# Kernel tuning notes

Hardware: AMD Instinct MI355X
Metric: run time of the kernel (lower is better)

The kernel has to match this reference:

```python
import jax, jax.numpy as jnp
import numpy as np
from jax import lax

B, S, IN, D, E, NH = 8, 128, 512, 1024, 4, 16
DH = D // NH
EPS = 1e-5
SCALE = np.float32(1.0 / np.sqrt(DH))


def setup_inputs() -> dict:
    key = jax.random.key(0)
    ks = iter(jax.random.split(key, 64))
    def rn(shape, scale=0.02):
        return jax.random.normal(next(ks), shape, dtype=jnp.float32) * scale
    z = lambda shape: jnp.zeros(shape, dtype=jnp.float32)
    return {
        "x": jax.random.normal(next(ks), (B, S, IN), dtype=jnp.float32),
        "router_w": rn((IN, E)), "router_b": z((E,)),
        "enc_w1": rn((E, IN, D)), "enc_b1": z((E, D)),
        "enc_w2": rn((E, D, D)), "enc_b2": z((E, D)),
        "enc_g": jnp.ones((E, D), jnp.float32), "enc_beta": z((E, D)),
        "attn_in_w": rn((E, D, 3 * D)), "attn_in_b": z((E, 3 * D)),
        "attn_out_w": rn((E, D, D)), "attn_out_b": z((E, D)),
        "lstm_wi_f": rn((E, D, 4 * D)), "lstm_wh_f": rn((E, D, 4 * D)), "lstm_b_f": z((E, 4 * D)),
        "lstm_wi_b": rn((E, D, 4 * D)), "lstm_wh_b": rn((E, D, 4 * D)), "lstm_b_b": z((E, 4 * D)),
        "sig_w1": rn((E, 2 * D, D)), "sig_b1": z((E, D)),
        "sig_w2": rn((E, D, D)), "sig_b2": z((E, D)),
        "tan_w1": rn((E, 2 * D, D)), "tan_b1": z((E, D)),
        "tan_w2": rn((E, D, D)), "tan_b2": z((E, D)),
        "dec_w1": rn((E, D, D)), "dec_b1": z((E, D)),
        "dec_w2": rn((E, D, IN)), "dec_b2": z((E, IN)),
        "dec_g": jnp.ones((E, IN), jnp.float32), "dec_beta": z((E, IN)),
    }


def _ln(x, g, b):
    m = x.mean(-1, keepdims=True)
    v = ((x - m) ** 2).mean(-1, keepdims=True)
    return (x - m) * lax.rsqrt(v + EPS) * g + b


def _lstm_dir(x, Wi, Wh, b):
    # x: [B,S,D]; single-direction LSTM, returns h sequence [B,S,H]
    bsz = x.shape[0]
    h0 = jnp.zeros((bsz, Wh.shape[0]), x.dtype)
    def step(carry, xt):
        h, c = carry
        zg = xt @ Wi + h @ Wh + b  # [B,4H]; torch gate order i,f,g,o
        i, f, g, o = jnp.split(zg, 4, axis=-1)
        c = jax.nn.sigmoid(f) * c + jax.nn.sigmoid(i) * jnp.tanh(g)
        h = jax.nn.sigmoid(o) * jnp.tanh(c)
        return (h, c), h
    _, hs = lax.scan(step, (h0, h0), jnp.swapaxes(x, 0, 1))
    return jnp.swapaxes(hs, 0, 1)


def _expert(x, p):
    (ew1, eb1, ew2, eb2, eg, ebeta, aiw, aib, aow, aob,
     wif, whf, bf, wibk, whbk, bbk, sw1, sb1, sw2, sb2,
     tw1, tb1, tw2, tb2, dw1, db1, dw2, db2, dg, dbeta) = p
    # encoder MLP + LayerNorm
    h = _ln(jax.nn.relu(x @ ew1 + eb1) @ ew2 + eb2, eg, ebeta)  # [B,S,D]
    # full self-attention (torch MultiheadAttention)
    qkv = h @ aiw + aib
    q, k, v = jnp.split(qkv, 3, axis=-1)
    def heads(t):
        return t.reshape(t.shape[0], t.shape[1], NH, DH).transpose(0, 2, 1, 3)
    q, k, v = heads(q), heads(k), heads(v)
    attn = jax.nn.softmax(jnp.einsum('bhqd,bhkd->bhqk', q, k) * SCALE, axis=-1)
    o = jnp.einsum('bhqk,bhkd->bhqd', attn, v).transpose(0, 2, 1, 3).reshape(h.shape)
    h = o @ aow + aob
    # bidirectional LSTM memory
    hf = _lstm_dir(h, wif, whf, bf)
    hb = _lstm_dir(h[:, ::-1], wibk, whbk, bbk)[:, ::-1]
    mem = jnp.concatenate([hf, hb], axis=-1)  # [B,S,2D]
    # sigmoid/tanh gate branches multiplied
    gate_s = jax.nn.sigmoid(jax.nn.relu(mem @ sw1 + sb1) @ sw2 + sb2)
    gate_t = jnp.tanh(jax.nn.relu(mem @ tw1 + tb1) @ tw2 + tb2)
    g = gate_s * gate_t  # [B,S,D]
    # decoder MLP + LayerNorm back to input_dim
    return _ln(jax.nn.relu(g @ dw1 + db1) @ dw2 + db2, dg, dbeta)


def _forward(x, router_w, router_b, *p):
    outs = jax.vmap(lambda pe: _expert(x, pe))(tuple(p))  # [E,B,S,IN]
    w = jax.nn.softmax(x @ router_w + router_b, axis=-1)  # [B,S,E] token-level routing
    return jnp.einsum('ebsd,bse->bsd', outs, w)


def reference(x, router_w, router_b, enc_w1, enc_b1, enc_w2, enc_b2, enc_g, enc_beta,
              attn_in_w, attn_in_b, attn_out_w, attn_out_b,
              lstm_wi_f, lstm_wh_f, lstm_b_f, lstm_wi_b, lstm_wh_b, lstm_b_b,
              sig_w1, sig_b1, sig_w2, sig_b2, tan_w1, tan_b1, tan_w2, tan_b2,
              dec_w1, dec_b1, dec_w2, dec_b2, dec_g, dec_beta):
    return _forward(x, router_w, router_b, enc_w1, enc_b1, enc_w2, enc_b2, enc_g, enc_beta,
                    attn_in_w, attn_in_b, attn_out_w, attn_out_b,
                    lstm_wi_f, lstm_wh_f, lstm_b_f, lstm_wi_b, lstm_wh_b, lstm_b_b,
                    sig_w1, sig_b1, sig_w2, sig_b2, tan_w1, tan_b1, tan_w2, tan_b2,
                    dec_w1, dec_b1, dec_w2, dec_b2, dec_g, dec_beta)
```

## Files before the change

### kernel.cpp

```cpp
#include <hip/hip_runtime.h>


typedef __attribute__((ext_vector_type(8))) short short8v;
typedef __attribute__((ext_vector_type(4))) float float4v;

__device__ __forceinline__ float bf2f(unsigned short u) {
    unsigned int x = ((unsigned int)u) << 16;
    return __builtin_bit_cast(float, x);
}
__device__ __forceinline__ unsigned short f2bf(float f) {
    unsigned int u = __builtin_bit_cast(unsigned int, f);
    u += 0x7fffu + ((u >> 16) & 1u);
    return (unsigned short)(u >> 16);
}
__device__ __forceinline__ void gload_lds16(const unsigned short* g, unsigned short* lds) {
    __builtin_amdgcn_global_load_lds(
        (const __attribute__((address_space(1))) unsigned int*)g,
        (__attribute__((address_space(3))) unsigned int*)lds, 16, 0, 0);
}
__device__ __forceinline__ float ftanh(float x) {
    float e = __expf(2.f * x);
    return 1.f - 2.f / (e + 1.f);
}

__global__ __launch_bounds__(256) void cvt_bf16_kernel(
    const float* __restrict__ in, unsigned short* __restrict__ out, int n4)
{
    int i = blockIdx.x * 256 + threadIdx.x;
    if (i >= n4) return;
    float4 v = *reinterpret_cast<const float4*>(&in[i * 4]);
    ushort4 o;
    o.x = f2bf(v.x); o.y = f2bf(v.y); o.z = f2bf(v.z); o.w = f2bf(v.w);
    *reinterpret_cast<ushort4*>(&out[i * 4]) = o;
}

struct TransJobs {
    const float* src[14];
    unsigned short* dst[14];
    int K[14], N[14];
    int prefix[15];
    long sWe[14], sTe[14];
};

__global__ __launch_bounds__(256) void transpose_all(TransJobs J)
{
    __shared__ float tile[64][33];
    int bid = blockIdx.x;
    int j = 0;
    #pragma unroll
    for (int i = 0; i < 14; ++i) if (bid >= J.prefix[i + 1]) j = i + 1;
    int lb = bid - J.prefix[j];
    int K = J.K[j], N = J.N[j];
    int tn = N >> 5, tk = K >> 6;
    int e = lb / (tn * tk), rem = lb % (tn * tk);
    int ky = rem / tn, nx = rem % tn;
    const float* W = J.src[j] + (long)e * J.sWe[j];
    unsigned short* Wt = J.dst[j] + (long)e * J.sTe[j];
    int k0 = ky * 64, n0 = nx * 32;
    int tx = threadIdx.x & 31, ty = threadIdx.x >> 5;
    #pragma unroll
    for (int i = 0; i < 64; i += 8)
        tile[ty + i][tx] = W[(long)(k0 + ty + i) * N + n0 + tx];
    __syncthreads();
    #pragma unroll
    for (int p = 0; p < 4; ++p) {
        int nn = ty + p * 8;
        unsigned lo = (unsigned)f2bf(tile[tx * 2][nn]);
        unsigned hi = (unsigned)f2bf(tile[tx * 2 + 1][nn]);
        *reinterpret_cast<unsigned*>(&Wt[(long)(n0 + nn) * K + k0 + tx * 2]) =
            lo | (hi << 16);
    }
}

__global__ __launch_bounds__(64) void router_kernel(
    const float* __restrict__ x, const float* __restrict__ rw,
    const float* __restrict__ rb, float* __restrict__ router)
{
    int token = blockIdx.x;
    int lane = threadIdx.x;
    float a0 = 0.f, a1 = 0.f, a2 = 0.f, a3 = 0.f;
    const float* xp = x + (long)token * 512;
    for (int i = lane; i < 512; i += 64) {
        float xv = xp[i];
        const float* w = rw + (long)i * 4;
        a0 += xv * w[0]; a1 += xv * w[1]; a2 += xv * w[2]; a3 += xv * w[3];
    }
    #pragma unroll
    for (int off = 32; off; off >>= 1) {
        a0 += __shfl_down(a0, off); a1 += __shfl_down(a1, off);
        a2 += __shfl_down(a2, off); a3 += __shfl_down(a3, off);
    }
    if (lane == 0) {
        a0 += rb[0]; a1 += rb[1]; a2 += rb[2]; a3 += rb[3];
        float m = fmaxf(fmaxf(a0, a1), fmaxf(a2, a3));
        float e0 = __expf(a0 - m), e1 = __expf(a1 - m);
        float e2 = __expf(a2 - m), e3 = __expf(a3 - m);
        float inv = 1.f / (e0 + e1 + e2 + e3);
        *reinterpret_cast<float4*>(&router[token * 4]) =
            make_float4(e0 * inv, e1 * inv, e2 * inv, e3 * inv);
    }
}

template <int OUTBF>
__global__ __launch_bounds__(512) void gemm_bf16(
    const unsigned short* __restrict__ A, const unsigned short* __restrict__ Wt,
    const float* __restrict__ bias, const float* __restrict__ bias2,
    const unsigned short* __restrict__ mul,
    void* __restrict__ Cv, int N, int K, int lda, int nsplit,
    long sAe, long sWe, long sBe, long sMe, long sCe, int act)
{
    __shared__ unsigned short As[2][128 * 64];
    __shared__ unsigned short Bs[2][128 * 64];
    int e = blockIdx.z;
    A += (long)e * sAe; Wt += (long)e * sWe;
    bias += (long)e * sBe; bias2 += (long)e * sBe;
    if (mul) mul += (long)e * sMe;
    int tid = threadIdx.x;
    int row0 = blockIdx.y * 128, col0 = blockIdx.x * 128;
    int wid = tid >> 6, lane = tid & 63;
    int wr = wid >> 2, wc = wid & 3;
    int l15 = lane & 15, l4 = lane >> 4;
    int r8 = lane >> 3, sg = lane & 7;
    float4v acc[4][2];
    #pragma unroll
    for (int i = 0; i < 4; ++i)
        #pragma unroll
        for (int j = 0; j < 2; ++j) acc[i][j] = (float4v){0.f, 0.f, 0.f, 0.f};

    auto STAGE = [&](int buf, int k0) {
        #pragma unroll
        for (int c = 0; c < 2; ++c) {
            int chunk = wid * 2 + c;
            int rowA = chunk * 8 + r8;
            int segA = (sg ^ (rowA & 7)) * 8;
            gload_lds16(A + (long)(row0 + rowA) * lda + k0 + segA,
                        (unsigned short*)((char*)As[buf] + chunk * 1024));
            gload_lds16(Wt + (long)(col0 + rowA) * K + k0 + segA,
                        (unsigned short*)((char*)Bs[buf] + chunk * 1024));
        }
    };
    int nt = K >> 6;
    STAGE(0, 0);
    asm volatile("s_waitcnt vmcnt(0)" ::: "memory");
    __builtin_amdgcn_s_barrier();
    for (int t = 0; t < nt; ++t) {
        int cur = t & 1;
        if (t + 1 < nt) STAGE(cur ^ 1, (t + 1) << 6);
        __builtin_amdgcn_sched_barrier(0);
        #pragma unroll
        for (int kk = 0; kk < 2; ++kk) {
            short8v af[4], bq[2];
            int bytec = kk * 64 + l4 * 16;
            #pragma unroll
            for (int m = 0; m < 4; ++m) {
                int r = wr * 64 + m * 16 + l15;
                af[m] = *reinterpret_cast<const short8v*>(
                    (char*)As[cur] + r * 128 + (bytec ^ ((r & 7) << 4)));
            }
            #pragma unroll
            for (int n = 0; n < 2; ++n) {
                int r = wc * 32 + n * 16 + l15;
                bq[n] = *reinterpret_cast<const short8v*>(
                    (char*)Bs[cur] + r * 128 + (bytec ^ ((r & 7) << 4)));
            }
            #pragma unroll
            for (int m = 0; m < 4; ++m)
                #pragma unroll
                for (int n = 0; n < 2; ++n)
                    acc[m][n] = __builtin_amdgcn_mfma_f32_16x16x32_bf16(
                        af[m], bq[n], acc[m][n], 0, 0, 0);
        }
        __builtin_amdgcn_sched_barrier(0);
        if (t + 1 < nt) {
            asm volatile("s_waitcnt vmcnt(0)" ::: "memory");
            __builtin_amdgcn_s_barrier();
        }
    }
    float* Cf = (float*)Cv + (long)e * sCe;
    unsigned short* Cb = (unsigned short*)Cv + (long)e * sCe;
    #pragma unroll
    for (int n = 0; n < 2; ++n) {
        int col = col0 + wc * 32 + n * 16 + l15;
        float bia = (col < nsplit) ? bias[col] : bias2[col - nsplit];
        #pragma unroll
        for (int m = 0; m < 4; ++m) {
            #pragma unroll
            for (int r = 0; r < 4; ++r) {
                long row = row0 + wr * 64 + m * 16 + l4 * 4 + r;
                float v = acc[m][n][r] + bia;
                if (act == 1) v = fmaxf(v, 0.f);
                else if (act == 2) v = 1.f / (1.f + __expf(-v));
                else if (act == 3) v = ftanh(v);
                if (mul) v *= bf2f(mul[row * N + col]);
                if (OUTBF) Cb[row * N + col] = f2bf(v);
                else       Cf[row * N + col] = v;
            }
        }
    }
}

template <int DIM>
__global__ __launch_bounds__(256) void ln_bf16(
    unsigned short* __restrict__ buf, const float* __restrict__ g,
    const float* __restrict__ beta)
{
    constexpr int PT = DIM / 256;
    __shared__ float sbuf[4];
    int row = blockIdx.x, e = row >> 10;
    unsigned short* p = buf + (long)row * DIM;
    const float* gp = g + (long)e * DIM;
    const float* bp = beta + (long)e * DIM;
    int tid = threadIdx.x;
    float v[PT];
    ushort4 u = *reinterpret_cast<const ushort4*>(p + tid * PT);
    v[0] = bf2f(u.x); v[1] = bf2f(u.y); v[2] = bf2f(u.z); v[3] = bf2f(u.w);
    float s = v[0] + v[1] + v[2] + v[3];
    #pragma unroll
    for (int off = 32; off; off >>= 1) s += __shfl_down(s, off);
    if ((tid & 63) == 0) sbuf[tid >> 6] = s;
    __syncthreads();
    float mean = (sbuf[0] + sbuf[1] + sbuf[2] + sbuf[3]) / (float)DIM;
    __syncthreads();
    float vs = 0.f;
    #pragma unroll
    for (int i = 0; i < PT; ++i) { float d = v[i] - mean; vs += d * d; }
    #pragma unroll
    for (int off = 32; off; off >>= 1) vs += __shfl_down(vs, off);
    if ((tid & 63) == 0) sbuf[tid >> 6] = vs;
    __syncthreads();
    float var = (sbuf[0] + sbuf[1] + sbuf[2] + sbuf[3]) / (float)DIM;
    float rstd = rsqrtf(var + 1e-5f);
    ushort4 o;
    o.x = f2bf((v[0] - mean) * rstd * gp[tid * PT + 0] + bp[tid * PT + 0]);
    o.y = f2bf((v[1] - mean) * rstd * gp[tid * PT + 1] + bp[tid * PT + 1]);
    o.z = f2bf((v[2] - mean) * rstd * gp[tid * PT + 2] + bp[tid * PT + 2]);
    o.w = f2bf((v[3] - mean) * rstd * gp[tid * PT + 3] + bp[tid * PT + 3]);
    *reinterpret_cast<ushort4*>(p + tid * PT) = o;
}

template <int DIM>
__global__ __launch_bounds__(256) void ln_kernel(
    float* __restrict__ buf, const float* __restrict__ g,
    const float* __restrict__ beta)
{
    constexpr int PT = DIM / 256;
    __shared__ float sbuf[4];
    int row = blockIdx.x, e = row >> 10;
    float* p = buf + (long)row * DIM;
    const float* gp = g + (long)e * DIM;
    const float* bp = beta + (long)e * DIM;
    int tid = threadIdx.x;
    float v[PT];
    float s = 0.f;
    #pragma unroll
    for (int i = 0; i < PT; ++i) { v[i] = p[tid + i * 256]; s += v[i]; }
    #pragma unroll
    for (int off = 32; off; off >>= 1) s += __shfl_down(s, off);
    if ((tid & 63) == 0) sbuf[tid >> 6] = s;
    __syncthreads();
    float mean = (sbuf[0] + sbuf[1] + sbuf[2] + sbuf[3]) / (float)DIM;
    __syncthreads();
    float vs = 0.f;
    #pragma unroll
    for (int i = 0; i < PT; ++i) { float d = v[i] - mean; vs += d * d; }
    #pragma unroll
    for (int off = 32; off; off >>= 1) vs += __shfl_down(vs, off);
    if ((tid & 63) == 0) sbuf[tid >> 6] = vs;
    __syncthreads();
    float var = (sbuf[0] + sbuf[1] + sbuf[2] + sbuf[3]) / (float)DIM;
    float rstd = rsqrtf(var + 1e-5f);
    #pragma unroll
    for (int i = 0; i < PT; ++i)
        p[tid + i * 256] = (v[i] - mean) * rstd * gp[tid + i * 256] + bp[tid + i * 256];
}

__global__ __launch_bounds__(128) void attn_bf16(
    const unsigned short* __restrict__ qkv, unsigned short* __restrict__ o)
{
    __shared__ __align__(16) float Ks[128][64];
    __shared__ __align__(16) float Vs[128][64];
    int id = blockIdx.x;
    int hd = id & 15, b = (id >> 4) & 7, e = id >> 7;
    int tid = threadIdx.x;
    const long base = ((long)e * 1024 + b * 128) * 3072 + hd * 64;
    #pragma unroll
    for (int i = 0; i < 8; ++i) {
        int idx = i * 128 + tid;
        int row = idx >> 3, f8 = (idx & 7) * 8;
        short8v kv = *reinterpret_cast<const short8v*>(&qkv[base + (long)row * 3072 + 1024 + f8]);
        short8v vv = *reinterpret_cast<const short8v*>(&qkv[base + (long)row * 3072 + 2048 + f8]);
        #pragma unroll
        for (int j = 0; j < 8; ++j) {
            Ks[row][f8 + j] = bf2f((unsigned short)kv[j]);
            Vs[row][f8 + j] = bf2f((unsigned short)vv[j]);
        }
    }
    __syncthreads();
    float q[64];
    #pragma unroll
    for (int f = 0; f < 8; ++f) {
        short8v qv = *reinterpret_cast<const short8v*>(&qkv[base + (long)tid * 3072 + f * 8]);
        #pragma unroll
        for (int j = 0; j < 8; ++j) q[f * 8 + j] = bf2f((unsigned short)qv[j]);
    }
    float m = -__builtin_huge_valf(), l = 0.f;
    float oa[64];
    #pragma unroll
    for (int d = 0; d < 64; ++d) oa[d] = 0.f;
    for (int j = 0; j < 128; ++j) {
        float s = 0.f;
        #pragma unroll
        for (int d = 0; d < 64; ++d) s = fmaf(q[d], Ks[j][d], s);
        s *= 0.125f;
        float mn = fmaxf(m, s);
        float corr = __expf(m - mn);
        float pj = __expf(s - mn);
        l = l * corr + pj;
        #pragma unroll
        for (int d = 0; d < 64; ++d) oa[d] = oa[d] * corr + pj * Vs[j][d];
        m = mn;
    }
    float inv = 1.f / l;
    unsigned short* op = o + ((long)e * 1024 + b * 128 + tid) * 1024 + hd * 64;
    #pragma unroll
    for (int f = 0; f < 8; ++f) {
        short8v ov;
        #pragma unroll
        for (int j = 0; j < 8; ++j) ov[j] = (short)f2bf(oa[f * 8 + j] * inv);
        *reinterpret_cast<short8v*>(&op[f * 8]) = ov;
    }
}

__global__ __launch_bounds__(512, 4) void lstm_persistent(
    const unsigned short* __restrict__ pre, const unsigned short* __restrict__ whtf,
    const unsigned short* __restrict__ whtb, unsigned short* __restrict__ hstate,
    unsigned short* __restrict__ memb, unsigned int* __restrict__ sync)
{
    __shared__ unsigned short hA[16 * 1024];
    __shared__ float zred[4][2][8][16];
    int bid = blockIdx.x;
    int ed = bid & 7, cb = bid >> 3;
    int e = ed >> 1, dir = ed & 1;
    const unsigned short* Wt = (dir ? whtb : whtf) + (long)e * 4096 * 1024;
    unsigned int* arr = sync + ed * 64;
    int tid = threadIdx.x;
    int w = tid >> 6, lane = tid & 63, l15 = lane & 15, l4 = lane >> 4;
    int g = w >> 1, kh = w & 1;
    short8v wf[16];
    const unsigned short* wp =
        Wt + ((long)(g * 1024 + cb * 16 + l15)) * 1024 + kh * 512 + l4 * 8;
    #pragma unroll
    for (int ks = 0; ks < 16; ++ks)
        wf[ks] = *reinterpret_cast<const short8v*>(wp + ks * 32);
    short8v z8 = {0, 0, 0, 0, 0, 0, 0, 0};
    for (int i = tid; i < 8 * 128; i += 512) {
        int r = 8 + (i >> 7), sb = (i & 127) * 16;
        *reinterpret_cast<short8v*>((char*)hA + r * 2048 + (sb ^ ((r & 7) << 4))) = z8;
    }
    float c0 = 0.f, c1 = 0.f;
    int gp = tid & 7, gb = tid >> 3;
    for (int s = 0; s < 128; ++s) {
        int t = dir ? 127 - s : s;
        const unsigned long long* hin64 = reinterpret_cast<const unsigned long long*>(
            hstate + (long)(s & 1) * 65536 + (long)ed * 8192);
        __syncthreads();
        #pragma unroll
        for (int i = 0; i < 4; ++i) {
            int idx = tid + 512 * i;
            unsigned long long v = __hip_atomic_load(
                hin64 + idx, __ATOMIC_RELAXED, __HIP_MEMORY_SCOPE_AGENT);
            int r = idx >> 8, sb = (idx & 255) * 8;
            *reinterpret_cast<unsigned long long*>(
                (char*)hA + r * 2048 + (sb ^ ((r & 7) << 4))) = v;
        }
        float pz[8];
        if (tid < 64) {
            const unsigned short* prow =
                pre + (((long)e * 1024) + gb * 128 + t) * 8192 + dir * 4096 + cb * 16 + gp * 2;
            #pragma unroll
            for (int gg = 0; gg < 4; ++gg) {
                unsigned int u = *reinterpret_cast<const unsigned int*>(prow + gg * 1024);
                pz[gg * 2]     = bf2f((unsigned short)(u & 0xffff));
                pz[gg * 2 + 1] = bf2f((unsigned short)(u >> 16));
            }
        }
        __syncthreads();
        float4v acc = (float4v){0.f, 0.f, 0.f, 0.f};
        int abase = l15 * 2048, aswz = (l15 & 7) << 4;
        #pragma unroll
        for (int ks = 0; ks < 16; ++ks) {
            short8v a = *reinterpret_cast<const short8v*>(
                (char*)hA + abase + (((kh * 512 + ks * 32) * 2 + l4 * 16) ^ aswz));
            acc = __builtin_amdgcn_mfma_f32_16x16x32_bf16(a, wf[ks], acc, 0, 0, 0);
        }
        if (l4 < 2) {
            #pragma unroll
            for (int r = 0; r < 4; ++r)
                zred[g][kh][l4 * 4 + r][l15] = acc[r];
        }
        __syncthreads();
        if (tid < 64) {
            int col0 = gp * 2;
            float h2[2];
            #pragma unroll
            for (int cc = 0; cc < 2; ++cc) {
                int col = col0 + cc;
                float zi = zred[0][0][gb][col] + zred[0][1][gb][col] + pz[0 + cc];
                float zf = zred[1][0][gb][col] + zred[1][1][gb][col] + pz[2 + cc];
                float zg = zred[2][0][gb][col] + zred[2][1][gb][col] + pz[4 + cc];
                float zo = zred[3][0][gb][col] + zred[3][1][gb][col] + pz[6 + cc];
                float ig = 1.f / (1.f + __expf(-zi));
                float fg = 1.f / (1.f + __expf(-zf));
                float gv = tanhf(zg);
                float og = 1.f / (1.f + __expf(-zo));
                float cv = cc ? c1 : c0;
                cv = fg * cv + ig * gv;
                if (cc) c1 = cv; else c0 = cv;
                h2[cc] = og * tanhf(cv);
            }
            unsigned int hv = (unsigned int)f2bf(h2[0]) | ((unsigned int)f2bf(h2[1]) << 16);
            int hcol = cb * 16 + col0;
            unsigned int* hout32 = reinterpret_cast<unsigned int*>(
                hstate + (long)((s & 1) ^ 1) * 65536 + (long)ed * 8192);
            __hip_atomic_store(hout32 + (gb * 1024 + hcol) / 2, hv,
                               __ATOMIC_RELAXED, __HIP_MEMORY_SCOPE_AGENT);
            *reinterpret_cast<unsigned int*>(
                memb + (((long)e * 8 + gb) * 128 + t) * 2048 + dir * 1024 + hcol) = hv;
        }
        if (s == 127) break;
        __syncthreads();
        if (tid == 0)
            __hip_atomic_store(arr + cb, (unsigned)(s + 1), __ATOMIC_RELAXED,
                               __HIP_MEMORY_SCOPE_AGENT);
        if (tid < 64) {
            while (__hip_atomic_load(arr + tid, __ATOMIC_RELAXED,
                                     __HIP_MEMORY_SCOPE_AGENT) < (unsigned)(s + 1))
                __builtin_amdgcn_s_sleep(1);
        }
    }
}

__global__ __launch_bounds__(256) void combine_kernel(
    const float* __restrict__ outs, const float* __restrict__ router,
    float* __restrict__ out)
{
    int idx = blockIdx.x * 256 + threadIdx.x;
    int token = idx >> 7, q = (idx & 127) * 4;
    float4 r = *reinterpret_cast<const float4*>(&router[token * 4]);
    const float* bp = outs + (long)token * 512 + q;
    float4 v0 = *reinterpret_cast<const float4*>(bp);
    float4 v1 = *reinterpret_cast<const float4*>(bp + 524288);
    float4 v2 = *reinterpret_cast<const float4*>(bp + 1048576);
    float4 v3 = *reinterpret_cast<const float4*>(bp + 1572864);
    float4 a;
    a.x = r.x * v0.x + r.y * v1.x + r.z * v2.x + r.w * v3.x;
    a.y = r.x * v0.y + r.y * v1.y + r.z * v2.y + r.w * v3.y;
    a.z = r.x * v0.z + r.y * v1.z + r.z * v2.z + r.w * v3.z;
    a.w = r.x * v0.w + r.y * v1.w + r.z * v2.w + r.w * v3.w;
    *reinterpret_cast<float4*>(&out[(long)token * 512 + q]) = a;
}

extern "C" void kernel_launch(void* const* d_in, const int* in_sizes, int n_in,
                              void* d_out, int out_size, void* d_ws, size_t ws_size,
                              hipStream_t stream)
{
    (void)in_sizes; (void)n_in; (void)out_size; (void)ws_size;
    const float* x        = (const float*)d_in[0];
    const float* router_w = (const float*)d_in[1];
    const float* router_b = (const float*)d_in[2];
    const float* enc_w1   = (const float*)d_in[3];
    const float* enc_b1   = (const float*)d_in[4];
    const float* enc_w2   = (const float*)d_in[5];
    const float* enc_b2   = (const float*)d_in[6];
    const float* enc_g    = (const float*)d_in[7];
    const float* enc_beta = (const float*)d_in[8];
    const float* aiw      = (const float*)d_in[9];
    const float* aib      = (const float*)d_in[10];
    const float* aow      = (const float*)d_in[11];
    const float* aob      = (const float*)d_in[12];
    const float* wif      = (const float*)d_in[13];
    const float* whf      = (const float*)d_in[14];
    const float* bfv      = (const float*)d_in[15];
    const float* wib      = (const float*)d_in[16];
    const float* whb      = (const float*)d_in[17];
    const float* bbv      = (const float*)d_in[18];
    const float* sw1      = (const float*)d_in[19];
    const float* sb1      = (const float*)d_in[20];
    const float* sw2      = (const float*)d_in[21];
    const float* sb2      = (const float*)d_in[22];
    const float* tw1      = (const float*)d_in[23];
    const float* tb1      = (const float*)d_in[24];
    const float* tw2      = (const float*)d_in[25];
    const float* tb2      = (const float*)d_in[26];
    const float* dw1      = (const float*)d_in[27];
    const float* db1      = (const float*)d_in[28];
    const float* dw2      = (const float*)d_in[29];
    const float* db2      = (const float*)d_in[30];
    const float* dg       = (const float*)d_in[31];
    const float* dbeta    = (const float*)d_in[32];
    float* out = (float*)d_out;

    const long m = 1024L * 1024L;
    unsigned short* U = (unsigned short*)d_ws;
    unsigned short* ew1T = U;
    unsigned short* ew2T = U + 2 * m;
    unsigned short* aiwT = U + 6 * m;
    unsigned short* aowT = U + 18 * m;
    unsigned short* wiT  = U + 22 * m;
    unsigned short* whtf = U + 54 * m;
    unsigned short* whtb = U + 70 * m;
    unsigned short* gw1T = U + 86 * m;
    unsigned short* sw2T = U + 102 * m;
    unsigned short* tw2T = U + 106 * m;
    unsigned short* dw1T = U + 110 * m;
    unsigned short* dw2T = U + 114 * m;
    unsigned short* xb   = U + 116 * m;
    unsigned short* hbuf = xb + 524288;
    unsigned short* t1   = hbuf + 4 * m;
    unsigned short* t2   = t1 + 4 * m;
    unsigned short* pre  = t2 + 4 * m;
    unsigned short* memb = pre + 32 * m;
    unsigned short* hstate = memb + 8 * m;
    float* F      = (float*)(U + 170 * m);
    float* outs   = F;
    float* router = outs + 2 * m;
    unsigned int* syncv = (unsigned int*)(router + 4096);

    hipMemsetAsync(hstate, 0, 65536 * sizeof(unsigned short), stream);
    hipMemsetAsync(syncv, 0, 1024 * sizeof(unsigned int), stream);

    cvt_bf16_kernel<<<512, 256, 0, stream>>>(x, xb, 131072);
    {
        TransJobs J;
        const float* srcs[14] = {enc_w1, enc_w2, aiw, aow, wif, wib, whf, whb,
                                 sw1, tw1, sw2, tw2, dw1, dw2};
        unsigned short* dsts[14] = {ew1T, ew2T, aiwT, aowT, wiT, wiT + 4096 * 1024L,
                                    whtf, whtb, gw1T, gw1T + 2 * m, sw2T, tw2T, dw1T, dw2T};
        int Ks[14] = {512, 1024, 1024, 1024, 1024, 1024, 1024, 1024,
                      2048, 2048, 1024, 1024, 1024, 1024};
        int Ns[14] = {1024, 1024, 3072, 1024, 4096, 4096, 4096, 4096,
                      1024, 1024, 1024, 1024, 1024, 512};
        long sWes[14] = {512 * 1024L, m, 3 * m, m, 4 * m, 4 * m, 4 * m, 4 * m,
                         2 * m, 2 * m, m, m, m, 512 * 1024L};
        long sTes[14] = {512 * 1024L, m, 3 * m, m, 8 * m, 8 * m, 4 * m, 4 * m,
                         4 * m, 4 * m, m, m, m, 512 * 1024L};
        int pfx = 0;
        J.prefix[0] = 0;
        for (int i = 0; i < 14; ++i) {
            J.src[i] = srcs[i]; J.dst[i] = dsts[i];
            J.K[i] = Ks[i]; J.N[i] = Ns[i];
            J.sWe[i] = sWes[i]; J.sTe[i] = sTes[i];
            pfx += (Ns[i] >> 5) * (Ks[i] >> 6) * 4;
            J.prefix[i + 1] = pfx;
        }
        transpose_all<<<pfx, 256, 0, stream>>>(J);
    }

    router_kernel<<<1024, 64, 0, stream>>>(x, router_w, router_b, router);

    gemm_bf16<1><<<dim3(8, 8, 4), 512, 0, stream>>>(xb, ew1T, enc_b1, enc_b1, nullptr, t1,
        1024, 512, 512, 1024, 0L, 512 * 1024L, 1024L, 0L, m, 1);
    gemm_bf16<1><<<dim3(8, 8, 4), 512, 0, stream>>>(t1, ew2T, enc_b2, enc_b2, nullptr, hbuf,
        1024, 1024, 1024, 1024, m, m, 1024L, 0L, m, 0);
    ln_bf16<1024><<<4096, 256, 0, stream>>>(hbuf, enc_g, enc_beta);
    gemm_bf16<1><<<dim3(24, 8, 4), 512, 0, stream>>>(hbuf, aiwT, aib, aib, nullptr, pre,
        3072, 1024, 1024, 3072, m, 3 * m, 3072L, 0L, 3 * m, 0);
    attn_bf16<<<512, 128, 0, stream>>>(pre, t1);
    gemm_bf16<1><<<dim3(8, 8, 4), 512, 0, stream>>>(t1, aowT, aob, aob, nullptr, hbuf,
        1024, 1024, 1024, 1024, m, m, 1024L, 0L, m, 0);
    gemm_bf16<1><<<dim3(64, 8, 4), 512, 0, stream>>>(hbuf, wiT, bfv, bbv, nullptr, pre,
        8192, 1024, 1024, 4096, m, 8 * m, 4096L, 0L, 8 * m, 0);
    lstm_persistent<<<512, 512, 0, stream>>>(pre, whtf, whtb, hstate, memb, syncv);
    unsigned short* g1o = pre;
    gemm_bf16<1><<<dim3(16, 8, 4), 512, 0, stream>>>(memb, gw1T, sb1, tb1, nullptr, g1o,
        2048, 2048, 2048, 1024, 2 * m, 4 * m, 1024L, 0L, 2 * m, 1);
    gemm_bf16<1><<<dim3(8, 8, 4), 512, 0, stream>>>(g1o, sw2T, sb2, sb2, nullptr, t2,
        1024, 1024, 2048, 1024, 2 * m, m, 1024L, 0L, m, 2);
    gemm_bf16<1><<<dim3(8, 8, 4), 512, 0, stream>>>(g1o + 1024, tw2T, tb2, tb2, t2, hbuf,
        1024, 1024, 2048, 1024, 2 * m, m, 1024L, m, m, 3);
    gemm_bf16<1><<<dim3(8, 8, 4), 512, 0, stream>>>(hbuf, dw1T, db1, db1, nullptr, t1,
        1024, 1024, 1024, 1024, m, m, 1024L, 0L, m, 1);
    gemm_bf16<0><<<dim3(4, 8, 4), 512, 0, stream>>>(t1, dw2T, db2, db2, nullptr, outs,
        512, 1024, 1024, 512, m, 512 * 1024L, 512L, 0L, 512 * 1024L, 0);
    ln_kernel<512><<<4096, 256, 0, stream>>>(outs, dg, dbeta);
    combine_kernel<<<512, 256, 0, stream>>>(outs, router, out);
}
```

Measured before the change: 1.203 ms.

## Widen LSTM persistent blocks to 64 hidden columns, cut grid to 128 blocks

Each persistent LSTM block now owns 64 hidden columns instead of 16, keeping four MFMA accumulator sets and 64 weight fragments in registers. The grid drops from 512 to 128 blocks, so each direction's barrier waits on 16 peers instead of 64. Sync counters are spaced 16 words apart to avoid false sharing. All 512 threads now compute gates, with lane shuffles packing bf16 pairs. The cost is much higher register pressure (launch bounds lowered to one block per CU), more serial MFMA work per block and fewer CUs in use.

Measured after the change: 1.534 ms. 27.5% more time.

```diff
diff --git a/kernel.cpp b/kernel.cpp
--- a/kernel.cpp
+++ b/kernel.cpp
@@ -331,34 +331,37 @@
     }
 }
 
-__global__ __launch_bounds__(512, 4) void lstm_persistent(
+__global__ __launch_bounds__(512, 1) void lstm_persistent(
     const unsigned short* __restrict__ pre, const unsigned short* __restrict__ whtf,
     const unsigned short* __restrict__ whtb, unsigned short* __restrict__ hstate,
     unsigned short* __restrict__ memb, unsigned int* __restrict__ sync)
 {
     __shared__ unsigned short hA[16 * 1024];
-    __shared__ float zred[4][2][8][16];
+    __shared__ float zred[4][2][8][64];
     int bid = blockIdx.x;
     int ed = bid & 7, cb = bid >> 3;
     int e = ed >> 1, dir = ed & 1;
     const unsigned short* Wt = (dir ? whtb : whtf) + (long)e * 4096 * 1024;
-    unsigned int* arr = sync + ed * 64;
+    unsigned int* arr = sync + ed * 256;
     int tid = threadIdx.x;
     int w = tid >> 6, lane = tid & 63, l15 = lane & 15, l4 = lane >> 4;
     int g = w >> 1, kh = w & 1;
-    short8v wf[16];
-    const unsigned short* wp =
-        Wt + ((long)(g * 1024 + cb * 16 + l15)) * 1024 + kh * 512 + l4 * 8;
-    #pragma unroll
-    for (int ks = 0; ks < 16; ++ks)
-        wf[ks] = *reinterpret_cast<const short8v*>(wp + ks * 32);
+    short8v wf[64];
+    #pragma unroll
+    for (int nf = 0; nf < 4; ++nf) {
+        const unsigned short* wp =
+            Wt + ((long)(g * 1024 + cb * 64 + nf * 16 + l15)) * 1024 + kh * 512 + l4 * 8;
+        #pragma unroll
+        for (int ks = 0; ks < 16; ++ks)
+            wf[nf * 16 + ks] = *reinterpret_cast<const short8v*>(wp + ks * 32);
+    }
     short8v z8 = {0, 0, 0, 0, 0, 0, 0, 0};
     for (int i = tid; i < 8 * 128; i += 512) {
         int r = 8 + (i >> 7), sb = (i & 127) * 16;
         *reinterpret_cast<short8v*>((char*)hA + r * 2048 + (sb ^ ((r & 7) << 4))) = z8;
     }
-    float c0 = 0.f, c1 = 0.f;
-    int gp = tid & 7, gb = tid >> 3;
+    float cval = 0.f;
+    int gb = tid >> 6, gcol = tid & 63;
     for (int s = 0; s < 128; ++s) {
         int t = dir ? 127 - s : s;
         const unsigned long long* hin64 = reinterpret_cast<const unsigned long long*>(
@@ -373,67 +376,66 @@
             *reinterpret_cast<unsigned long long*>(
                 (char*)hA + r * 2048 + (sb ^ ((r & 7) << 4))) = v;
         }
-        float pz[8];
-        if (tid < 64) {
+        float pz[4];
+        {
             const unsigned short* prow =
-                pre + (((long)e * 1024) + gb * 128 + t) * 8192 + dir * 4096 + cb * 16 + gp * 2;
-            #pragma unroll
-            for (int gg = 0; gg < 4; ++gg) {
-                unsigned int u = *reinterpret_cast<const unsigned int*>(prow + gg * 1024);
-                pz[gg * 2]     = bf2f((unsigned short)(u & 0xffff));
-                pz[gg * 2 + 1] = bf2f((unsigned short)(u >> 16));
-            }
+                pre + (((long)e * 1024) + gb * 128 + t) * 8192 + dir * 4096 + cb * 64 + gcol;
+            #pragma unroll
+            for (int gg = 0; gg < 4; ++gg) pz[gg] = bf2f(prow[gg * 1024]);
         }
         __syncthreads();
-        float4v acc = (float4v){0.f, 0.f, 0.f, 0.f};
+        float4v acc[4];
+        #pragma unroll
+        for (int nf = 0; nf < 4; ++nf) acc[nf] = (float4v){0.f, 0.f, 0.f, 0.f};
         int abase = l15 * 2048, aswz = (l15 & 7) << 4;
         #pragma unroll
         for (int ks = 0; ks < 16; ++ks) {
             short8v a = *reinterpret_cast<const short8v*>(
                 (char*)hA + abase + (((kh * 512 + ks * 32) * 2 + l4 * 16) ^ aswz));
-            acc = __builtin_amdgcn_mfma_f32_16x16x32_bf16(a, wf[ks], acc, 0, 0, 0);
+            #pragma unroll
+            for (int nf = 0; nf < 4; ++nf)
+                acc[nf] = __builtin_amdgcn_mfma_f32_16x16x32_bf16(
+                    a, wf[nf * 16 + ks], acc[nf], 0, 0, 0);
         }
         if (l4 < 2) {
             #pragma unroll
-            for (int r = 0; r < 4; ++r)
-                zred[g][kh][l4 * 4 + r][l15] = acc[r];
+            for (int nf = 0; nf < 4; ++nf)
+                #pragma unroll
+                for (int r = 0; r < 4; ++r)
+                    zred[g][kh][l4 * 4 + r][nf * 16 + l15] = acc[nf][r];
         }
         __syncthreads();
-        if (tid < 64) {
-            int col0 = gp * 2;
-            float h2[2];
-            #pragma unroll
-            for (int cc = 0; cc < 2; ++cc) {
-                int col = col0 + cc;
-                float zi = zred[0][0][gb][col] + zred[0][1][gb][col] + pz[0 + cc];
-                float zf = zred[1][0][gb][col] + zred[1][1][gb][col] + pz[2 + cc];
-                float zg = zred[2][0][gb][col] + zred[2][1][gb][col] + pz[4 + cc];
-                float zo = zred[3][0][gb][col] + zred[3][1][gb][col] + pz[6 + cc];
-                float ig = 1.f / (1.f + __expf(-zi));
-                float fg = 1.f / (1.f + __expf(-zf));
-                float gv = tanhf(zg);
-                float og = 1.f / (1.f + __expf(-zo));
-                float cv = cc ? c1 : c0;
-                cv = fg * cv + ig * gv;
-                if (cc) c1 = cv; else c0 = cv;
-                h2[cc] = og * tanhf(cv);
+        {
+            float zi = zred[0][0][gb][gcol] + zred[0][1][gb][gcol] + pz[0];
+            float zf = zred[1][0][gb][gcol] + zred[1][1][gb][gcol] + pz[1];
+            float zg = zred[2][0][gb][gcol] + zred[2][1][gb][gcol] + pz[2];
+            float zo = zred[3][0][gb][gcol] + zred[3][1][gb][gcol] + pz[3];
+            float ig = 1.f / (1.f + __expf(-zi));
+            float fg = 1.f / (1.f + __expf(-zf));
+            float gv = tanhf(zg);
+            float og = 1.f / (1.f + __expf(-zo));
+            cval = fg * cval + ig * gv;
+            float h = og * tanhf(cval);
+            unsigned short hb = f2bf(h);
+            unsigned partner = (unsigned)(unsigned short)__shfl_xor((int)hb, 1);
+            if ((gcol & 1) == 0) {
+                unsigned hv = (unsigned)hb | (partner << 16);
+                int hcol = cb * 64 + gcol;
+                unsigned int* hout32 = reinterpret_cast<unsigned int*>(
+                    hstate + (long)((s & 1) ^ 1) * 65536 + (long)ed * 8192);
+                __hip_atomic_store(hout32 + (gb * 1024 + hcol) / 2, hv,
+                                   __ATOMIC_RELAXED, __HIP_MEMORY_SCOPE_AGENT);
+                *reinterpret_cast<unsigned int*>(
+                    memb + (((long)e * 8 + gb) * 128 + t) * 2048 + dir * 1024 + hcol) = hv;
             }
-            unsigned int hv = (unsigned int)f2bf(h2[0]) | ((unsigned int)f2bf(h2[1]) << 16);
-            int hcol = cb * 16 + col0;
-            unsigned int* hout32 = reinterpret_cast<unsigned int*>(
-                hstate + (long)((s & 1) ^ 1) * 65536 + (long)ed * 8192);
-            __hip_atomic_store(hout32 + (gb * 1024 + hcol) / 2, hv,
-                               __ATOMIC_RELAXED, __HIP_MEMORY_SCOPE_AGENT);
-            *reinterpret_cast<unsigned int*>(
-                memb + (((long)e * 8 + gb) * 128 + t) * 2048 + dir * 1024 + hcol) = hv;
         }
         if (s == 127) break;
         __syncthreads();
         if (tid == 0)
-            __hip_atomic_store(arr + cb, (unsigned)(s + 1), __ATOMIC_RELAXED,
+            __hip_atomic_store(arr + cb * 16, (unsigned)(s + 1), __ATOMIC_RELAXED,
                                __HIP_MEMORY_SCOPE_AGENT);
-        if (tid < 64) {
-            while (__hip_atomic_load(arr + tid, __ATOMIC_RELAXED,
+        if (tid < 16) {
+            while (__hip_atomic_load(arr + tid * 16, __ATOMIC_RELAXED,
                                      __HIP_MEMORY_SCOPE_AGENT) < (unsigned)(s + 1))
                 __builtin_amdgcn_s_sleep(1);
         }
@@ -527,7 +529,7 @@
     unsigned int* syncv = (unsigned int*)(router + 4096);
 
     hipMemsetAsync(hstate, 0, 65536 * sizeof(unsigned short), stream);
-    hipMemsetAsync(syncv, 0, 1024 * sizeof(unsigned int), stream);
+    hipMemsetAsync(syncv, 0, 4096 * sizeof(unsigned int), stream);
 
     cvt_bf16_kernel<<<512, 256, 0, stream>>>(x, xb, 131072);
     {
@@ -570,7 +572,7 @@
         1024, 1024, 1024, 1024, m, m, 1024L, 0L, m, 0);
     gemm_bf16<1><<<dim3(64, 8, 4), 512, 0, stream>>>(hbuf, wiT, bfv, bbv, nullptr, pre,
         8192, 1024, 1024, 4096, m, 8 * m, 4096L, 0L, 8 * m, 0);
-    lstm_persistent<<<512, 512, 0, stream>>>(pre, whtf, whtb, hstate, memb, syncv);
+    lstm_persistent<<<128, 512, 0, stream>>>(pre, whtf, whtb, hstate, memb, syncv);
     unsigned short* g1o = pre;
     gemm_bf16<1><<<dim3(16, 8, 4), 512, 0, stream>>>(memb, gw1T, sb1, tb1, nullptr, g1o,
         2048, 2048, 2048, 1024, 2 * m, 4 * m, 1024L, 0L, 2 * m, 1);
```
